# Kernel tuning notes

Hardware: AMD Instinct MI355X
Metric: run time of the kernel (lower is better)

The kernel has to match this reference:

```python
import jax, jax.numpy as jnp
import numpy as np

NE, NM, NR = 32768, 65536, 49152   # enzyme / metabolite / reaction node counts
E = 262144                          # edges per relation
H, HEADS, DH, FFN, EF = 128, 4, 32, 512, 8


def setup_inputs():
    key = jax.random.key(0)
    ks = iter(jax.random.split(key, 64))
    def nrm(shape, s=1.0):
        return jax.random.normal(next(ks), shape, jnp.float32) * s
    def idx(n):
        return jax.random.randint(next(ks), (E,), 0, n, jnp.int32)
    w = 0.02
    return {
        'h_enz': nrm((NE, H)), 'h_met': nrm((NM, H)), 'h_rxn': nrm((NR, H)),
        'ef_mod': nrm((E, EF)), 'ef_sig': nrm((E, EF)),
        'ef_brg': nrm((E, EF)), 'ef_trn': nrm((E, EF)),
        'ln1_g': jnp.ones((3, H)), 'ln1_b': jnp.zeros((3, H)),
        'ln2_g': jnp.ones((3, H)), 'ln2_b': jnp.zeros((3, H)),
        'wp': nrm((3, H, H), w), 'bp': jnp.zeros((3, H)),
        'wl': nrm((5, H, H), w), 'a_src': nrm((5, HEADS, DH), w), 'a_dst': nrm((5, HEADS, DH), w),
        'we': nrm((4, EF, H), w), 'a_edge': nrm((4, HEADS, DH), w),
        'w1': nrm((3, H, FFN), w), 'b1': jnp.zeros((3, FFN)),
        'w2': nrm((3, FFN, H), w), 'b2': jnp.zeros((3, H)),
        'src_sub': idx(NM), 'dst_sub': idx(NR),    # metabolite -substrate_of-> reaction
        'src_prod': idx(NR), 'dst_prod': idx(NM),  # reaction -produces-> metabolite
        'src_cat': idx(NE), 'dst_cat': idx(NR),    # enzyme -catalyzes-> reaction
        'src_mod': idx(NE), 'dst_mod': idx(NR),    # enzyme -modulates-> reaction
        'src_reg': idx(NE), 'dst_reg': idx(NE),    # enzyme -regulates-> enzyme
        'src_sig': idx(NM), 'dst_sig': idx(NE),    # metabolite -signaling-> enzyme
        'src_brg': idx(NM), 'dst_brg': idx(NM),    # metabolite -bridges-> metabolite
        'src_trn': idx(NM), 'dst_trn': idx(NM),    # metabolite -transports_to-> metabolite
    }


def _ln(x, g, b, eps=1e-5):
    m = jnp.mean(x, -1, keepdims=True)
    v = jnp.mean((x - m) ** 2, -1, keepdims=True)
    return g * (x - m) * jax.lax.rsqrt(v + eps) + b


def _phys(h_src, src, dst, nd, w, b):
    # KineticConv: linear transform of source feats, mean-aggregated onto dst nodes
    msg = (h_src @ w + b)[src]                                  # [E, H]
    s = jax.ops.segment_sum(msg, dst, num_segments=nd)
    deg = jax.ops.segment_sum(jnp.ones((src.shape[0], 1), msg.dtype), dst, num_segments=nd)
    return s / jnp.maximum(deg, 1.0)


def _gat(h_src, h_dst, src, dst, nd, w, a_s, a_d, ef=None, w_e=None, a_e=None):
    # LearnedConv: multi-head GAT, optional edge features added to attention logits
    zs = (h_src @ w).reshape(-1, HEADS, DH)                     # [Ns, H', D]
    zd = (h_dst @ w).reshape(-1, HEADS, DH)                     # [Nd, H', D]
    logit = jnp.einsum('nhd,hd->nh', zs, a_s)[src] + jnp.einsum('nhd,hd->nh', zd, a_d)[dst]
    if ef is not None:
        ze = (ef @ w_e).reshape(-1, HEADS, DH)
        logit = logit + jnp.einsum('ehd,hd->eh', ze, a_e)
    logit = jax.nn.leaky_relu(logit, 0.2)                       # [E, H']
    m = jax.ops.segment_max(logit, dst, num_segments=nd)
    ex = jnp.exp(logit - m[dst])
    den = jax.ops.segment_sum(ex, dst, num_segments=nd)
    alpha = ex / jnp.maximum(den[dst], 1e-9)                    # segment softmax over incoming edges
    out = jax.ops.segment_sum(alpha[:, :, None] * zs[src], dst, num_segments=nd)
    return out.reshape(nd, H)                                   # concat heads -> H


def reference(h_enz, h_met, h_rxn, ef_mod, ef_sig, ef_brg, ef_trn,
              ln1_g, ln1_b, ln2_g, ln2_b, wp, bp, wl, a_src, a_dst, we, a_edge,
              w1, b1, w2, b2,
              src_sub, dst_sub, src_prod, dst_prod, src_cat, dst_cat,
              src_mod, dst_mod, src_reg, dst_reg, src_sig, dst_sig,
              src_brg, dst_brg, src_trn, dst_trn):
    # ntype index: 0=enzyme 1=metabolite 2=reaction. Dropout = identity (eval mode).
    ne = _ln(h_enz, ln1_g[0], ln1_b[0])
    nm = _ln(h_met, ln1_g[1], ln1_b[1])
    nr = _ln(h_rxn, ln1_g[2], ln1_b[2])
    m_rxn = [
        _phys(nm, src_sub, dst_sub, NR, wp[0], bp[0]),
        _phys(ne, src_cat, dst_cat, NR, wp[2], bp[2]),
        _gat(ne, nr, src_mod, dst_mod, NR, wl[0], a_src[0], a_dst[0], ef_mod, we[0], a_edge[0]),
    ]
    m_met = [
        _phys(nr, src_prod, dst_prod, NM, wp[1], bp[1]),
        _gat(nm, nm, src_brg, dst_brg, NM, wl[3], a_src[3], a_dst[3], ef_brg, we[2], a_edge[2]),
        _gat(nm, nm, src_trn, dst_trn, NM, wl[4], a_src[4], a_dst[4], ef_trn, we[3], a_edge[3]),
    ]
    m_enz = [
        _gat(ne, ne, src_reg, dst_reg, NE, wl[1], a_src[1], a_dst[1]),
        _gat(nm, ne, src_sig, dst_sig, NE, wl[2], a_src[2], a_dst[2], ef_sig, we[1], a_edge[1]),
    ]
    # stack + mean aggregation across relations, then residual
    h_e = h_enz + sum(m_enz) / float(len(m_enz))
    h_m = h_met + sum(m_met) / float(len(m_met))
    h_r = h_rxn + sum(m_rxn) / float(len(m_rxn))
    # Pre-LN FFN per node type: h + W2 GELU(W1 LN(h))
    def ffn(h, i):
        n = _ln(h, ln2_g[i], ln2_b[i])
        return h + (jax.nn.gelu(n @ w1[i] + b1[i], approximate=False) @ w2[i] + b2[i])
    return jnp.concatenate([ffn(h_e, 0), ffn(h_m, 1), ffn(h_r, 2)], axis=0)
```

## Files before the change

kernel.cpp:

```cpp
#include <hip/hip_runtime.h>
#include <cstddef>

#define NE 32768
#define NM 65536
#define NR 49152
#define NTOT 147456
#define E2 262144
#define NDPAD 65536
#define RPS 65537
#define W1T_OFF 131072
#define W2T_OFF 327680

typedef __attribute__((ext_vector_type(8))) short bf16x8;
typedef __attribute__((ext_vector_type(4))) float f32x4;
typedef __attribute__((ext_vector_type(2))) float f32x2;

__device__ __forceinline__ unsigned short f2bf(float x) {
    unsigned u = __float_as_uint(x);
    return (unsigned short)((u + 0x7FFFu + ((u >> 16) & 1u)) >> 16);
}
__device__ __forceinline__ float bf2f(unsigned s) { return __uint_as_float(s << 16); }
__device__ __forceinline__ unsigned pk2(float a, float b) {
    return (unsigned)f2bf(a) | ((unsigned)f2bf(b) << 16);
}
__device__ __forceinline__ bf16x8 pack8(const float* v) {
    union { bf16x8 b; unsigned u[4]; } r;
#pragma unroll
    for (int i = 0; i < 4; ++i) r.u[i] = pk2(v[2 * i], v[2 * i + 1]);
    return r.b;
}
__device__ __forceinline__ bf16x8 pack8v(f32x4 a, f32x4 b) {
    union { bf16x8 v; unsigned u[4]; } r;
    r.u[0] = pk2(a[0], a[1]); r.u[1] = pk2(a[2], a[3]);
    r.u[2] = pk2(b[0], b[1]); r.u[3] = pk2(b[2], b[3]);
    return r.v;
}
__device__ __forceinline__ unsigned short pkfp8(float a, float b) {
    return (unsigned short)__builtin_amdgcn_cvt_pk_fp8_f32(a, b, 0u, false);
}
__device__ __forceinline__ void gll16(const void* g, void* l) {
    __builtin_amdgcn_global_load_lds(
        (const __attribute__((address_space(1))) void*)g,
        (__attribute__((address_space(3))) void*)l, 16, 0, 0);
}

__global__ __launch_bounds__(256) void convw(
    const float* __restrict__ wp, const float* __restrict__ wl,
    const float* __restrict__ w1, const float* __restrict__ w2,
    unsigned short* __restrict__ wbf)
{
    int i = blockIdx.x * 256 + threadIdx.x;
    float v;
    if (i < 131072) {
        int mat = i >> 14, r = i & 16383;
        int frag = r >> 9, lane = (r >> 3) & 63, j = r & 7;
        int nf = frag >> 2, ks = frag & 3;
        int n = nf * 16 + (lane & 15);
        int k = ks * 32 + (lane >> 4) * 8 + j;
        const float* src = (mat < 3) ? (wp + mat * 16384) : (wl + (mat - 3) * 16384);
        v = src[k * 128 + n];
    } else if (i < 327680) {
        int ii = i - 131072; int mat = ii >> 16, r = ii & 65535;
        int frag = r >> 9, lane = (r >> 3) & 63, j = r & 7;
        int nf = frag >> 2, ks = frag & 3;
        int n = nf * 16 + (lane & 15);
        int k = ks * 32 + (lane >> 4) * 8 + j;
        v = w1[mat * 65536 + k * 512 + n];
    } else {
        int ii = i - 327680; int mat = ii >> 16, r = ii & 65535;
        int frag = r >> 9, lane = (r >> 3) & 63, j = r & 7;
        int ks = frag >> 3, nf = frag & 7;
        int n = nf * 16 + (lane & 15);
        int k = ks * 32 + (lane >> 4) * 8 + j;
        v = w2[mat * 65536 + k * 128 + n];
    }
    wbf[i] = f2bf(v);
}

__global__ __launch_bounds__(256) void wqk(
    const float* __restrict__ wl, const float* __restrict__ a_src,
    const float* __restrict__ a_dst, unsigned short* __restrict__ wq)
{
    const int wi[7]  = {0, 2, 0, 1, 2, 3, 4};
    const int loi[7] = {0, 2, 0, 1, 2, 3, 4};
    const int lod[7] = {1, 1, 0, 0, 0, 0, 0};
    const int hii[7] = {-1, -1, -1, 1, -1, 3, 4};
    int site = blockIdx.x >> 2, ks = blockIdx.x & 3, t = threadIdx.x;
    const float* W = wl + wi[site] * 16384;
#pragma unroll
    for (int rep = 0; rep < 2; ++rep) {
        int e = t * 2 + rep;
        int lane = e >> 3, j = e & 7;
        int n = lane & 15;
        int k = ks * 32 + (lane >> 4) * 8 + j;
        float v = 0.f;
        if (n < 4) {
            const float* a = (lod[site] ? a_dst : a_src) + loi[site] * 128;
#pragma unroll 8
            for (int d = 0; d < 32; ++d) v += W[k * 128 + n * 32 + d] * a[n * 32 + d];
        } else if (n < 8 && hii[site] >= 0) {
            const float* a = a_dst + hii[site] * 128;
            int hh = n - 4;
#pragma unroll 8
            for (int d = 0; d < 32; ++d) v += W[k * 128 + hh * 32 + d] * a[hh * 32 + d];
        }
        wq[((site * 4 + ks) * 64 + lane) * 8 + j] = f2bf(v);
    }
}

__global__ __launch_bounds__(256) void ln1_kernel(
    const float* __restrict__ he, const float* __restrict__ hm, const float* __restrict__ hr,
    const float* __restrict__ g, const float* __restrict__ b, unsigned* __restrict__ nout)
{
    int row  = blockIdx.x * 4 + (threadIdx.x >> 6);
    int lane = threadIdx.x & 63;
    const float* src; int ti; int lr;
    if (row < NE)           { src = he; ti = 0; lr = row; }
    else if (row < NE + NM) { src = hm; ti = 1; lr = row - NE; }
    else                    { src = hr; ti = 2; lr = row - NE - NM; }
    float2 x = *(const float2*)(src + (size_t)lr * 128 + lane * 2);
    float s = x.x + x.y;
#pragma unroll
    for (int o = 32; o; o >>= 1) s += __shfl_xor(s, o);
    float mean = s * (1.0f / 128.0f);
    float dx = x.x - mean, dy = x.y - mean;
    float v = dx * dx + dy * dy;
#pragma unroll
    for (int o = 32; o; o >>= 1) v += __shfl_xor(v, o);
    float rstd = rsqrtf(v * (1.0f / 128.0f) + 1e-5f);
    int c = lane * 2;
    float y0 = g[ti * 128 + c]     * dx * rstd + b[ti * 128 + c];
    float y1 = g[ti * 128 + c + 1] * dy * rstd + b[ti * 128 + c + 1];
    nout[(size_t)row * 64 + lane] = pk2(y0, y1);
}

template <int LOG, bool BIAS>
__global__ __launch_bounds__(256) void gemm_v2(
    const unsigned short* __restrict__ A, const unsigned short* __restrict__ Wt,
    const float* __restrict__ bias, unsigned short* __restrict__ Zp,
    const unsigned short* __restrict__ WQ, float* __restrict__ oa, float* __restrict__ ob)
{
    __shared__ unsigned short WL[16384];
    int t = threadIdx.x, w = t >> 6, l = t & 63;
    int l15 = l & 15, lq = l >> 4;
#pragma unroll
    for (int i = 0; i < 8; ++i)
        gll16(Wt + i * 2048 + t * 8, (char*)WL + i * 4096 + t * 16);
    size_t row0 = (size_t)blockIdx.x * 128 + w * 32;
    f32x4 acc[2][8]; f32x4 accl[2];
#pragma unroll
    for (int r = 0; r < 2; ++r) {
        accl[r] = (f32x4){0.f, 0.f, 0.f, 0.f};
#pragma unroll
        for (int n = 0; n < 8; ++n) acc[r][n] = (f32x4){0.f, 0.f, 0.f, 0.f};
    }
    bf16x8 qf[4];
    if constexpr (LOG >= 1) {
#pragma unroll
        for (int ks = 0; ks < 4; ++ks) qf[ks] = *(const bf16x8*)(WQ + (ks * 64 + l) * 8);
    }
    __syncthreads();
#pragma unroll
    for (int ks = 0; ks < 4; ++ks) {
        int k0 = ks * 32 + lq * 8;
        bf16x8 a0 = *(const bf16x8*)(A + (row0 + l15) * 128 + k0);
        bf16x8 a1 = *(const bf16x8*)(A + (row0 + 16 + l15) * 128 + k0);
#pragma unroll
        for (int n = 0; n < 8; ++n) {
            bf16x8 bw = *(const bf16x8*)(WL + ((n * 4 + ks) * 64 + l) * 8);
            acc[0][n] = __builtin_amdgcn_mfma_f32_16x16x32_bf16(a0, bw, acc[0][n], 0, 0, 0);
            acc[1][n] = __builtin_amdgcn_mfma_f32_16x16x32_bf16(a1, bw, acc[1][n], 0, 0, 0);
        }
        if constexpr (LOG >= 1) {
            accl[0] = __builtin_amdgcn_mfma_f32_16x16x32_bf16(a0, qf[ks], accl[0], 0, 0, 0);
            accl[1] = __builtin_amdgcn_mfma_f32_16x16x32_bf16(a1, qf[ks], accl[1], 0, 0, 0);
        }
    }
#pragma unroll
    for (int n = 0; n < 4; ++n) {
        float bl = BIAS ? bias[n * 16 + l15] : 0.f;
        float bh = BIAS ? bias[n * 16 + l15 + 64] : 0.f;
#pragma unroll
        for (int r = 0; r < 2; ++r)
#pragma unroll
            for (int reg = 0; reg < 4; ++reg) {
                size_t row = row0 + r * 16 + lq * 4 + reg;
                Zp[row * 64 + n * 16 + l15] = pkfp8(acc[r][n][reg] + bl, acc[r][n + 4][reg] + bh);
            }
    }
    if constexpr (LOG >= 1) {
#pragma unroll
        for (int r = 0; r < 2; ++r)
#pragma unroll
            for (int reg = 0; reg < 4; ++reg) {
                size_t row = row0 + r * 16 + lq * 4 + reg;
                if (l15 < 4) oa[row * 4 + l15] = accl[r][reg];
                else if (LOG == 2 && l15 < 8) ob[row * 4 + (l15 - 4)] = accl[r][reg];
            }
    }
}

struct P8 { const int* a[8]; };
#define CHUNK 2048

__global__ __launch_bounds__(256) void bucket_count(P8 dsts, unsigned* __restrict__ bcnt)
{
    __shared__ unsigned lh[256];
    int blk = blockIdx.x, rel = blk >> 7, cb = blk & 127, t = threadIdx.x;
    lh[t] = 0; __syncthreads();
    const int* dp = dsts.a[rel] + cb * CHUNK;
#pragma unroll
    for (int it = 0; it < 8; ++it) atomicAdd(&lh[dp[it * 256 + t] >> 8], 1u);
    __syncthreads();
    atomicAdd(&bcnt[rel * 256 + t], lh[t]);
}

__global__ __launch_bounds__(256) void scanB(const unsigned* __restrict__ bcnt,
                                             unsigned* __restrict__ bbase,
                                             unsigned* __restrict__ bcur)
{
    __shared__ unsigned ts[256];
    int t = threadIdx.x;
    unsigned v[8]; unsigned run = 0;
#pragma unroll
    for (int i = 0; i < 8; ++i) { v[i] = bcnt[t * 8 + i]; run += v[i]; }
    ts[t] = run; __syncthreads();
    for (int off = 1; off < 256; off <<= 1) {
        unsigned x = (t >= off) ? ts[t - off] : 0u;
        __syncthreads(); ts[t] += x; __syncthreads();
    }
    unsigned base = ts[t] - run;
#pragma unroll
    for (int i = 0; i < 8; ++i) { bbase[t * 8 + i] = base; bcur[t * 8 + i] = base; base += v[i]; }
    if (t == 255) bbase[2048] = base;
}

__global__ __launch_bounds__(256) void bucket_fill(P8 dsts, P8 srcs,
                                                   unsigned* __restrict__ bcur,
                                                   unsigned long long* __restrict__ bb)
{
    __shared__ unsigned lh[256], lbase[256], lcur[256];
    int blk = blockIdx.x, rel = blk >> 7, cb = blk & 127, t = threadIdx.x;
    lh[t] = 0; lcur[t] = 0; __syncthreads();
    const int* dp = dsts.a[rel] + cb * CHUNK;
    const int* sp = srcs.a[rel] + cb * CHUNK;
    int dv[8];
#pragma unroll
    for (int it = 0; it < 8; ++it) { dv[it] = dp[it * 256 + t]; atomicAdd(&lh[dv[it] >> 8], 1u); }
    __syncthreads();
    lbase[t] = atomicAdd(&bcur[rel * 256 + t], lh[t]);
    __syncthreads();
#pragma unroll
    for (int it = 0; it < 8; ++it) {
        unsigned e = (unsigned)(cb * CHUNK + it * 256 + t);
        unsigned d = (unsigned)dv[it];
        unsigned s = (unsigned)sp[it * 256 + t];
        unsigned pos = atomicAdd(&lcur[d >> 8], 1u);
        bb[lbase[d >> 8] + pos] =
            (unsigned long long)s | ((unsigned long long)d << 16) | ((unsigned long long)e << 32);
    }
}

__global__ __launch_bounds__(256) void bucket_hist(const unsigned long long* __restrict__ bb,
                                                   const unsigned* __restrict__ bbase,
                                                   unsigned* __restrict__ hist)
{
    __shared__ unsigned lh[256];
    int blk = blockIdx.x, rel = blk >> 8, b = blk & 255, t = threadIdx.x;
    lh[t] = 0; __syncthreads();
    unsigned s0 = bbase[blk], s1 = bbase[blk + 1];
    for (unsigned i = s0 + t; i < s1; i += 256)
        atomicAdd(&lh[(unsigned)(bb[i] >> 16) & 255u], 1u);
    __syncthreads();
    hist[(size_t)rel * NDPAD + b * 256 + t] = lh[t];
}

__global__ __launch_bounds__(256) void scan1(const unsigned* __restrict__ hist,
                                             unsigned* __restrict__ rowptr,
                                             unsigned* __restrict__ blksum)
{
    __shared__ unsigned s[256];
    int b = blockIdx.x, rel = b >> 8, c = b & 255, t = threadIdx.x;
    unsigned v = hist[(size_t)rel * NDPAD + c * 256 + t];
    s[t] = v; __syncthreads();
    for (int off = 1; off < 256; off <<= 1) {
        unsigned x = (t >= off) ? s[t - off] : 0u;
        __syncthreads();
        s[t] += x;
        __syncthreads();
    }
    rowptr[(size_t)rel * RPS + c * 256 + t] = s[t] - v;
    if (t == 255) blksum[rel * 256 + c] = s[255];
}

__global__ __launch_bounds__(256) void scan2(unsigned* __restrict__ blksum,
                                             unsigned* __restrict__ rowptr)
{
    __shared__ unsigned s[256];
    int rel = blockIdx.x, t = threadIdx.x;
    unsigned v = blksum[rel * 256 + t];
    s[t] = v; __syncthreads();
    for (int off = 1; off < 256; off <<= 1) {
        unsigned x = (t >= off) ? s[t - off] : 0u;
        __syncthreads();
        s[t] += x;
        __syncthreads();
    }
    blksum[rel * 256 + t] = s[t] - v;
    if (t == 255) rowptr[(size_t)rel * RPS + 65536] = s[255];
}

__global__ __launch_bounds__(256) void scan3(unsigned* __restrict__ rowptr,
                                             const unsigned* __restrict__ blksum)
{
    int b = blockIdx.x, rel = b >> 8, c = b & 255, t = threadIdx.x;
    rowptr[(size_t)rel * RPS + c * 256 + t] += blksum[rel * 256 + c];
}

__global__ __launch_bounds__(256) void bucket_place(const unsigned long long* __restrict__ bb,
                                                    const unsigned* __restrict__ bbase,
                                                    const unsigned* __restrict__ rowptr,
                                                    int2* __restrict__ epair)
{
    __shared__ unsigned lrp[256], lcur[256];
    int blk = blockIdx.x, rel = blk >> 8, b = blk & 255, t = threadIdx.x;
    lrp[t] = rowptr[(size_t)rel * RPS + b * 256 + t];
    lcur[t] = 0; __syncthreads();
    unsigned s0 = bbase[blk], s1 = bbase[blk + 1];
    for (unsigned i = s0 + t; i < s1; i += 256) {
        unsigned long long pk = bb[i];
        unsigned s = (unsigned)pk & 0xffffu;
        unsigned d8 = (unsigned)(pk >> 16) & 255u;
        unsigned e = (unsigned)(pk >> 32);
        unsigned pos = atomicAdd(&lcur[d8], 1u);
        epair[(size_t)rel * E2 + lrp[d8] + pos] = make_int2((int)s, (int)e);
    }
}

__global__ __launch_bounds__(256) void ef4e_kernel(
    const float* __restrict__ efm, const float* __restrict__ efs,
    const float* __restrict__ efb, const float* __restrict__ eft,
    const float* __restrict__ we, const float* __restrict__ ae,
    uint2* __restrict__ ef4e)
{
    __shared__ float M[8][4];
    int b = blockIdx.x, t = threadIdx.x;
    int er = b >> 10;
    const float* ef = (er == 0) ? efm : (er == 1) ? efs : (er == 2) ? efb : eft;
    if (t < 32) {
        int f = t >> 2, hh = t & 3;
        float s = 0.f;
#pragma unroll 8
        for (int d = 0; d < 32; ++d) s += we[er * 1024 + f * 128 + hh * 32 + d] * ae[er * 128 + hh * 32 + d];
        M[f][hh] = s;
    }
    __syncthreads();
    int e = (b & 1023) * 256 + t;
    float4 a = *(const float4*)(ef + (size_t)e * 8);
    float4 c = *(const float4*)(ef + (size_t)e * 8 + 4);
    float o0 = a.x*M[0][0]+a.y*M[1][0]+a.z*M[2][0]+a.w*M[3][0]+c.x*M[4][0]+c.y*M[5][0]+c.z*M[6][0]+c.w*M[7][0];
// ... 152 lines not shown
    unsigned* __restrict__ accp, int n_nodes)
{
    int t = threadIdx.x;
    unsigned m = (unsigned)(t & 15);
    int d = blockIdx.x * 16 + (t >> 4);
    if (d >= n_nodes) return;
    int hs = (int)(m >> 3);
    float rlo[4] = {0, 0, 0, 0}, rhi[4] = {0, 0, 0, 0};
    gat_seg16<EF>(rowptr, epair, Zp, ls, ld, ef4e, d, m, hs, rlo, rhi);
    acc_write16(accp, d, m, ACC, rlo, rhi);
}

template <bool EFA, bool EFB, bool ACC>
__global__ __launch_bounds__(256) void dual_gat(
    const unsigned* __restrict__ rpA, const int2* __restrict__ epA,
    const unsigned short* __restrict__ ZA, const float* __restrict__ lsA,
    const float* __restrict__ ldA, const uint2* __restrict__ efA,
    const unsigned* __restrict__ rpB, const int2* __restrict__ epB,
    const unsigned short* __restrict__ ZB, const float* __restrict__ lsB,
    const float* __restrict__ ldB, const uint2* __restrict__ efB,
    unsigned* __restrict__ accp, int n_nodes)
{
    int t = threadIdx.x;
    unsigned m = (unsigned)(t & 15);
    int d = blockIdx.x * 16 + (t >> 4);
    if (d >= n_nodes) return;
    int hs = (int)(m >> 3);
    float rlo[4] = {0, 0, 0, 0}, rhi[4] = {0, 0, 0, 0};
    gat_seg16<EFA>(rpA, epA, ZA, lsA, ldA, efA, d, m, hs, rlo, rhi);
    gat_seg16<EFB>(rpB, epB, ZB, lsB, ldB, efB, d, m, hs, rlo, rhi);
    acc_write16(accp, d, m, ACC, rlo, rhi);
}

__global__ __launch_bounds__(256, 2) void ffn_v5(
    const float* __restrict__ h, const unsigned* __restrict__ accp,
    const float* __restrict__ g, const float* __restrict__ b,
    const unsigned short* __restrict__ w1t, const float* __restrict__ b1,
    const unsigned short* __restrict__ w2t, const float* __restrict__ b2,
    float* __restrict__ out, float invC)
{
    __shared__ unsigned short WB[2][16384];
    __shared__ float HW[4][1024];
    int t = threadIdx.x, w = t >> 6, l = t & 63;
    int l15 = l & 15, lq = l >> 4;
    size_t rw = (size_t)blockIdx.x * 128 + w * 32;
    float* myHW = HW[w];

    bf16x8 af[2][4];
#pragma unroll
    for (int rf = 0; rf < 2; ++rf) {
        size_t myrow = rw + rf * 16 + l15;
        const unsigned* ap = accp + myrow * 64 + lq * 8;
        uint4 ua0 = *(const uint4*)(ap);
        uint4 ua1 = *(const uint4*)(ap + 4);
        uint4 ub0 = *(const uint4*)(ap + 32);
        uint4 ub1 = *(const uint4*)(ap + 36);
        const float* hp = h + myrow * 128 + lq * 8;
        float4 hf[4][2];
        hf[0][0] = *(const float4*)(hp);      hf[0][1] = *(const float4*)(hp + 4);
        hf[1][0] = *(const float4*)(hp + 32); hf[1][1] = *(const float4*)(hp + 36);
        hf[2][0] = *(const float4*)(hp + 64); hf[2][1] = *(const float4*)(hp + 68);
        hf[3][0] = *(const float4*)(hp + 96); hf[3][1] = *(const float4*)(hp + 100);
        unsigned ua[8] = {ua0.x, ua0.y, ua0.z, ua0.w, ua1.x, ua1.y, ua1.z, ua1.w};
        unsigned ub[8] = {ub0.x, ub0.y, ub0.z, ub0.w, ub1.x, ub1.y, ub1.z, ub1.w};
        float hv[4][8];
#pragma unroll
        for (int j = 0; j < 8; ++j) {
            hv[0][j] = ((const float*)hf[0])[j] + bf2f(ua[j] & 0xffffu) * invC;
            hv[1][j] = ((const float*)hf[1])[j] + bf2f(ub[j] & 0xffffu) * invC;
            hv[2][j] = ((const float*)hf[2])[j] + bf2f(ua[j] >> 16) * invC;
            hv[3][j] = ((const float*)hf[3])[j] + bf2f(ub[j] >> 16) * invC;
        }
        float s = 0.f;
#pragma unroll
        for (int ks = 0; ks < 4; ++ks)
#pragma unroll
            for (int j = 0; j < 8; ++j) s += hv[ks][j];
        s += __shfl_xor(s, 16); s += __shfl_xor(s, 32);
// ... 32 lines not shown
    int swR = (l15 & 7) << 2;
    for (int ch = 0; ch < 8; ++ch) {
        if (ch < 7) {
            const unsigned short* s1p = w1t + (ch + 1) * 8192;
            const unsigned short* s2p = w2t + (ch + 1) * 8192;
#pragma unroll
            for (int i = 0; i < 4; ++i) {
                gll16(s1p + i * 2048 + t * 8, (char*)WB[buf ^ 1] + i * 4096 + t * 16);
                gll16(s2p + i * 2048 + t * 8, (char*)WB[buf ^ 1] + 16384 + i * 4096 + t * 16);
            }
        }
        f32x4 acc1[2][4];
#pragma unroll
        for (int rf = 0; rf < 2; ++rf)
#pragma unroll
            for (int n = 0; n < 4; ++n) acc1[rf][n] = (f32x4){0.f, 0.f, 0.f, 0.f};
#pragma unroll
        for (int ks = 0; ks < 4; ++ks)
#pragma unroll
            for (int nf = 0; nf < 4; ++nf) {
                bf16x8 bw = *(const bf16x8*)(WB[buf] + ((nf * 4 + ks) * 64 + l) * 8);
                acc1[0][nf] = __builtin_amdgcn_mfma_f32_16x16x32_bf16(af[0][ks], bw, acc1[0][nf], 0, 0, 0);
                acc1[1][nf] = __builtin_amdgcn_mfma_f32_16x16x32_bf16(af[1][ks], bw, acc1[1][nf], 0, 0, 0);
            }
#pragma unroll
        for (int rf = 0; rf < 2; ++rf) {
#pragma unroll
            for (int nf = 0; nf < 4; ++nf) {
                float bv = b1[ch * 64 + nf * 16 + l15];
#pragma unroll
                for (int reg = 0; reg < 4; ++reg) {
                    int row = lq * 4 + reg;
                    float x = acc1[rf][nf][reg] + bv;
                    float ge = 0.5f * x * (1.0f + erff(x * 0.70710678118654752f));
                    myHW[row * 64 + ((nf * 16 + l15) ^ ((row & 7) << 2))] = ge;
                }
            }
#pragma unroll
            for (int ks2 = 0; ks2 < 2; ++ks2) {
                int cb = ks2 * 32 + lq * 8;
                f32x4 x0 = *(const f32x4*)(myHW + l15 * 64 + (cb ^ swR));
                f32x4 x1 = *(const f32x4*)(myHW + l15 * 64 + ((cb + 4) ^ swR));
                bf16x8 a2 = pack8v(x0, x1);
#pragma unroll
                for (int nf = 0; nf < 8; ++nf) {
                    bf16x8 bw = *(const bf16x8*)(WB[buf] + 8192 + ((ks2 * 8 + nf) * 64 + l) * 8);
                    facc[rf][nf] = __builtin_amdgcn_mfma_f32_16x16x32_bf16(a2, bw, facc[rf][nf], 0, 0, 0);
                }
            }
        }
        __syncthreads();
        buf ^= 1;
    }
#pragma unroll
    for (int rf = 0; rf < 2; ++rf)
#pragma unroll
        for (int nf = 0; nf < 8; ++nf) {
            int col = nf * 16 + l15;
            float bv = b2[col];
            int ci = col & 63;
            bool hi = col >= 64;
#pragma unroll
            for (int reg = 0; reg < 4; ++reg) {
                size_t row = rw + rf * 16 + lq * 4 + reg;
                unsigned pv = accp[row * 64 + ci];
                float av = bf2f(hi ? (pv >> 16) : (pv & 0xffffu));
                out[row * 128 + col] = h[row * 128 + col] + av * invC + facc[rf][nf][reg] + bv;
            }
// ... 20 lines not shown
    const float* wl     = (const float*)d_in[13];
    const float* a_src  = (const float*)d_in[14];
    const float* a_dst  = (const float*)d_in[15];
    const float* we     = (const float*)d_in[16];
    const float* a_edge = (const float*)d_in[17];
    const float* w1     = (const float*)d_in[18];
    const float* b1     = (const float*)d_in[19];
    const float* w2     = (const float*)d_in[20];
    const float* b2     = (const float*)d_in[21];
    const int* src_sub  = (const int*)d_in[22];
    const int* dst_sub  = (const int*)d_in[23];
    const int* src_prod = (const int*)d_in[24];
    const int* dst_prod = (const int*)d_in[25];
    const int* src_cat  = (const int*)d_in[26];
    const int* dst_cat  = (const int*)d_in[27];
    const int* src_mod  = (const int*)d_in[28];
    const int* dst_mod  = (const int*)d_in[29];
    const int* src_reg  = (const int*)d_in[30];
    const int* dst_reg  = (const int*)d_in[31];
    const int* src_sig  = (const int*)d_in[32];
    const int* dst_sig  = (const int*)d_in[33];
    const int* src_brg  = (const int*)d_in[34];
    const int* dst_brg  = (const int*)d_in[35];
    const int* src_trn  = (const int*)d_in[36];
    const int* dst_trn  = (const int*)d_in[37];
    float* out = (float*)d_out;

    char* p = (char*)d_ws;
    unsigned* accp = (unsigned*)p;            p += (size_t)NTOT * 64 * 4;
    unsigned short* ZpA = (unsigned short*)p; p += (size_t)NM * 64 * 2;
    unsigned long long* bukbuf = (unsigned long long*)p;
    unsigned short* ZpB = (unsigned short*)p; p += (size_t)8 * E2 * 8;
    int2* epair = (int2*)p;                   p += (size_t)8 * E2 * 8;
    unsigned* hist = (unsigned*)p;
    uint2* ef4e = (uint2*)p;                  p += (size_t)4 * E2 * 8;
    float* ls3 = (float*)p;                   p += (size_t)NE * 4 * 4;
    float* ld3 = (float*)p;                   p += (size_t)NR * 4 * 4;
    float* ls4 = (float*)p;                   p += (size_t)NE * 4 * 4;
    float* ld4 = (float*)p;                   p += (size_t)NE * 4 * 4;
    float* ls5 = (float*)p;                   p += (size_t)NM * 4 * 4;
    float* ld5 = (float*)p;                   p += (size_t)NE * 4 * 4;
    float* ls6 = (float*)p;                   p += (size_t)NM * 4 * 4;
    float* ld6 = (float*)p;                   p += (size_t)NM * 4 * 4;
    float* ls7 = (float*)p;                   p += (size_t)NM * 4 * 4;
    float* ld7 = (float*)p;                   p += (size_t)NM * 4 * 4;
    unsigned short* wbf = (unsigned short*)p; p += (size_t)524288 * 2;
    unsigned short* wq  = (unsigned short*)p; p += (size_t)7 * 2048 * 2;
    unsigned* rowptr = (unsigned*)p;          p += (size_t)8 * RPS * 4;
    unsigned* bcnt = (unsigned*)p;            p += 2048 * 4;
    unsigned* bbase = (unsigned*)p;           p += 2049 * 4;
    unsigned* bcur = (unsigned*)p;            p += 2048 * 4;
    unsigned* blksum = (unsigned*)p;          p += (size_t)8 * 256 * 4;
    if (ws_size < (size_t)(p - (char*)d_ws)) return;

    unsigned* nrm32 = (unsigned*)d_out;
    const unsigned short* nbf_enz = (const unsigned short*)d_out;
    const unsigned short* nbf_met = nbf_enz + (size_t)NE * 128;
    const unsigned short* nbf_rxn = nbf_enz + (size_t)(NE + NM) * 128;
    unsigned* acc_enz = accp;
    unsigned* acc_met = accp + (size_t)NE * 64;
    unsigned* acc_rxn = accp + (size_t)(NE + NM) * 64;

    P8 dsts, srcs;
    dsts.a[0] = dst_sub;  srcs.a[0] = src_sub;
    dsts.a[1] = dst_prod; srcs.a[1] = src_prod;
    dsts.a[2] = dst_cat;  srcs.a[2] = src_cat;
    dsts.a[3] = dst_mod;  srcs.a[3] = src_mod;
    dsts.a[4] = dst_reg;  srcs.a[4] = src_reg;
    dsts.a[5] = dst_sig;  srcs.a[5] = src_sig;
    dsts.a[6] = dst_brg;  srcs.a[6] = src_brg;
    dsts.a[7] = dst_trn;  srcs.a[7] = src_trn;

    hipMemsetAsync(bcnt, 0, 2048 * 4, stream);
    convw<<<2048, 256, 0, stream>>>(wp, wl, w1, w2, wbf);
    ln1_kernel<<<NTOT / 4, 256, 0, stream>>>(h_enz, h_met, h_rxn, ln1_g, ln1_b, nrm32);
    wqk<<<28, 256, 0, stream>>>(wl, a_src, a_dst, wq);
    bucket_count<<<1024, 256, 0, stream>>>(dsts, bcnt);
    scanB<<<1, 256, 0, stream>>>(bcnt, bbase, bcur);
    bucket_fill<<<1024, 256, 0, stream>>>(dsts, srcs, bcur, bukbuf);
    bucket_hist<<<2048, 256, 0, stream>>>(bukbuf, bbase, hist);
    scan1<<<2048, 256, 0, stream>>>(hist, rowptr, blksum);
    scan2<<<8, 256, 0, stream>>>(blksum, rowptr);
    scan3<<<2048, 256, 0, stream>>>(rowptr, blksum);
    bucket_place<<<2048, 256, 0, stream>>>(bukbuf, bbase, rowptr, epair);
    ef4e_kernel<<<4096, 256, 0, stream>>>(ef_mod, ef_sig, ef_brg, ef_trn, we, a_edge, ef4e);

#define RP(r) (rowptr + (size_t)(r) * RPS)
#define EP(r) (epair + (size_t)(r) * E2)
#define WQS(s) (wq + (size_t)(s) * 2048)
#define EF4(er) (ef4e + (size_t)(er) * E2)

    gemm_v2<0, true><<<NM / 128, 256, 0, stream>>>(nbf_met, wbf + 0 * 16384, bp + 0, ZpA,
                                                   nullptr, nullptr, nullptr);
    gemm_v2<1, true><<<NE / 128, 256, 0, stream>>>(nbf_enz, wbf + 2 * 16384, bp + 256, ZpB,
                                                   WQS(1), ld5, nullptr);
    dual_phys<false><<<NR / 16, 256, 0, stream>>>(RP(0), EP(0), ZpA, RP(2), EP(2), ZpB,
                                                  acc_rxn, NR);
    gemm_v2<1, true><<<NR / 128, 256, 0, stream>>>(nbf_rxn, wbf + 1 * 16384, bp + 128, ZpA,
                                                   WQS(0), ld3, nullptr);
    phys_gather<false><<<NM / 16, 256, 0, stream>>>(RP(1), EP(1), ZpA, acc_met, NM);
    gemm_v2<1, false><<<NE / 128, 256, 0, stream>>>(nbf_enz, wbf + 3 * 16384, nullptr, ZpB,
                                                    WQS(2), ls3, nullptr);
    gat_gather<true, true><<<NR / 16, 256, 0, stream>>>(RP(3), EP(3), ZpB, ls3, ld3, EF4(0),
                                                        acc_rxn, NR);
    gemm_v2<2, false><<<NE / 128, 256, 0, stream>>>(nbf_enz, wbf + 4 * 16384, nullptr, ZpA,
                                                    WQS(3), ls4, ld4);
    gemm_v2<1, false><<<NM / 128, 256, 0, stream>>>(nbf_met, wbf + 5 * 16384, nullptr, ZpB,
                                                    WQS(4), ls5, nullptr);
    dual_gat<false, true, false><<<NE / 16, 256, 0, stream>>>(
        RP(4), EP(4), ZpA, ls4, ld4, nullptr,
        RP(5), EP(5), ZpB, ls5, ld5, EF4(1), acc_enz, NE);
    gemm_v2<2, false><<<NM / 128, 256, 0, stream>>>(nbf_met, wbf + 6 * 16384, nullptr, ZpA,
                                                    WQS(5), ls6, ld6);
    gemm_v2<2, false><<<NM / 128, 256, 0, stream>>>(nbf_met, wbf + 7 * 16384, nullptr, ZpB,
                                                    WQS(6), ls7, ld7);
    dual_gat<true, true, true><<<NM / 16, 256, 0, stream>>>(
        RP(6), EP(6), ZpA, ls6, ld6, EF4(2),
        RP(7), EP(7), ZpB, ls7, ld7, EF4(3), acc_met, NM);

    ffn_v5<<<NE / 128, 256, 0, stream>>>(h_enz, acc_enz, ln2_g + 0, ln2_b + 0,
                                         wbf + W1T_OFF + 0 * 65536, b1 + 0,
                                         wbf + W2T_OFF + 0 * 65536, b2 + 0,
                                         out + 0, 0.5f);
    ffn_v5<<<NM / 128, 256, 0, stream>>>(h_met, acc_met, ln2_g + 128, ln2_b + 128,
                                         wbf + W1T_OFF + 1 * 65536, b1 + 512,
                                         wbf + W2T_OFF + 1 * 65536, b2 + 128,
                                         out + (size_t)NE * 128, 1.0f / 3.0f);
    ffn_v5<<<NR / 128, 256, 0, stream>>>(h_rxn, acc_rxn, ln2_g + 256, ln2_b + 256,
                                         wbf + W1T_OFF + 2 * 65536, b1 + 1024,
                                         wbf + W2T_OFF + 2 * 65536, b2 + 256,
                                         out + (size_t)(NE + NM) * 128, 1.0f / 3.0f);
#undef RP
#undef EP
#undef WQS
#undef EF4
}
```

Baseline: 469.4 us.

## Merge prep, CSR-build, GEMM and FFN launches and use tanh-form GELU

Folds ln1, weight conversion and the attention-logit weight prep into a single prep kernel. It merges histogram with scan1 and scan3 with placement, pairs independent projection GEMMs into one launch each, and runs all three FFNs in one grid. This cuts launch count and drops the intermediate hist buffer round-trip. Separately, the exact erf GELU is replaced by a sigmoid-based tanh approximation, which is cheaper but changes numerics slightly. The GEMM's compile-time LOG/BIAS branches become runtime pointer checks, adding some branching and register pressure.

```diff
diff --git a/kernel.cpp b/kernel.cpp
--- a/kernel.cpp
+++ b/kernel.cpp
@@ -6,10 +6,11 @@
 #define NR 49152
 #define NTOT 147456
 #define E2 262144
-#define NDPAD 65536
 #define RPS 65537
 #define W1T_OFF 131072
 #define W2T_OFF 327680
+#define LN1_BLK 36864
+#define CONV_BLK 2048
 
 typedef __attribute__((ext_vector_type(8))) short bf16x8;
 typedef __attribute__((ext_vector_type(4))) float f32x4;
@@ -43,110 +44,126 @@
         (const __attribute__((address_space(1))) void*)g,
         (__attribute__((address_space(3))) void*)l, 16, 0, 0);
 }
-
-__global__ __launch_bounds__(256) void convw(
+__device__ __forceinline__ float gelu(float x) {
+    float y = x * (1.5957691216f + 0.0713548163f * (x * x));
+    float e = __expf(-y);
+    return x / (1.0f + e);
+}
+
+__global__ __launch_bounds__(256) void prep_all(
+    const float* __restrict__ he, const float* __restrict__ hm, const float* __restrict__ hr,
+    const float* __restrict__ g1, const float* __restrict__ b1g, unsigned* __restrict__ nout,
     const float* __restrict__ wp, const float* __restrict__ wl,
     const float* __restrict__ w1, const float* __restrict__ w2,
-    unsigned short* __restrict__ wbf)
-{
-    int i = blockIdx.x * 256 + threadIdx.x;
-    float v;
-    if (i < 131072) {
-        int mat = i >> 14, r = i & 16383;
-        int frag = r >> 9, lane = (r >> 3) & 63, j = r & 7;
-        int nf = frag >> 2, ks = frag & 3;
-        int n = nf * 16 + (lane & 15);
-        int k = ks * 32 + (lane >> 4) * 8 + j;
-        const float* src = (mat < 3) ? (wp + mat * 16384) : (wl + (mat - 3) * 16384);
-        v = src[k * 128 + n];
-    } else if (i < 327680) {
-        int ii = i - 131072; int mat = ii >> 16, r = ii & 65535;
-        int frag = r >> 9, lane = (r >> 3) & 63, j = r & 7;
-        int nf = frag >> 2, ks = frag & 3;
-        int n = nf * 16 + (lane & 15);
-        int k = ks * 32 + (lane >> 4) * 8 + j;
-        v = w1[mat * 65536 + k * 512 + n];
+    unsigned short* __restrict__ wbf,
+    const float* __restrict__ a_src, const float* __restrict__ a_dst,
+    unsigned short* __restrict__ wq)
+{
+    int blk = blockIdx.x, t = threadIdx.x;
+    if (blk < LN1_BLK) {
+        int row  = blk * 4 + (t >> 6);
+        int lane = t & 63;
+        const float* src; int ti; int lr;
+        if (row < NE)           { src = he; ti = 0; lr = row; }
+        else if (row < NE + NM) { src = hm; ti = 1; lr = row - NE; }
+        else                    { src = hr; ti = 2; lr = row - NE - NM; }
+        float2 x = *(const float2*)(src + (size_t)lr * 128 + lane * 2);
+        float s = x.x + x.y;
+#pragma unroll
+        for (int o = 32; o; o >>= 1) s += __shfl_xor(s, o);
+        float mean = s * (1.0f / 128.0f);
+        float dx = x.x - mean, dy = x.y - mean;
+        float v = dx * dx + dy * dy;
+#pragma unroll
+        for (int o = 32; o; o >>= 1) v += __shfl_xor(v, o);
+        float rstd = rsqrtf(v * (1.0f / 128.0f) + 1e-5f);
+        int c = lane * 2;
+        float y0 = g1[ti * 128 + c]     * dx * rstd + b1g[ti * 128 + c];
+        float y1 = g1[ti * 128 + c + 1] * dy * rstd + b1g[ti * 128 + c + 1];
+        nout[(size_t)row * 64 + lane] = pk2(y0, y1);
+    } else if (blk < LN1_BLK + CONV_BLK) {
+        int i = (blk - LN1_BLK) * 256 + t;
+        float v;
+        if (i < 131072) {
+            int mat = i >> 14, r = i & 16383;
+            int frag = r >> 9, lane = (r >> 3) & 63, j = r & 7;
+            int nf = frag >> 2, ks = frag & 3;
+            int n = nf * 16 + (lane & 15);
+            int k = ks * 32 + (lane >> 4) * 8 + j;
+            const float* src = (mat < 3) ? (wp + mat * 16384) : (wl + (mat - 3) * 16384);
+            v = src[k * 128 + n];
+        } else if (i < 327680) {
+            int ii = i - 131072; int mat = ii >> 16, r = ii & 65535;
+            int frag = r >> 9, lane = (r >> 3) & 63, j = r & 7;
+            int nf = frag >> 2, ks = frag & 3;
+            int n = nf * 16 + (lane & 15);
+            int k = ks * 32 + (lane >> 4) * 8 + j;
+            v = w1[mat * 65536 + k * 512 + n];
+        } else {
+            int ii = i - 327680; int mat = ii >> 16, r = ii & 65535;
+            int frag = r >> 9, lane = (r >> 3) & 63, j = r & 7;
+            int ks = frag >> 3, nf = frag & 7;
+            int n = nf * 16 + (lane & 15);
+            int k = ks * 32 + (lane >> 4) * 8 + j;
+            v = w2[mat * 65536 + k * 128 + n];
+        }
+        wbf[i] = f2bf(v);
     } else {
-        int ii = i - 327680; int mat = ii >> 16, r = ii & 65535;
-        int frag = r >> 9, lane = (r >> 3) & 63, j = r & 7;
-        int ks = frag >> 3, nf = frag & 7;
-        int n = nf * 16 + (lane & 15);
-        int k = ks * 32 + (lane >> 4) * 8 + j;
-        v = w2[mat * 65536 + k * 128 + n];
-    }
-    wbf[i] = f2bf(v);
-}
-
-__global__ __launch_bounds__(256) void wqk(
-    const float* __restrict__ wl, const float* __restrict__ a_src,
-    const float* __restrict__ a_dst, unsigned short* __restrict__ wq)
-{
-    const int wi[7]  = {0, 2, 0, 1, 2, 3, 4};
-    const int loi[7] = {0, 2, 0, 1, 2, 3, 4};
-    const int lod[7] = {1, 1, 0, 0, 0, 0, 0};
-    const int hii[7] = {-1, -1, -1, 1, -1, 3, 4};
-    int site = blockIdx.x >> 2, ks = blockIdx.x & 3, t = threadIdx.x;
-    const float* W = wl + wi[site] * 16384;
-#pragma unroll
-    for (int rep = 0; rep < 2; ++rep) {
-        int e = t * 2 + rep;
-        int lane = e >> 3, j = e & 7;
-        int n = lane & 15;
-        int k = ks * 32 + (lane >> 4) * 8 + j;
-        float v = 0.f;
-        if (n < 4) {
-            const float* a = (lod[site] ? a_dst : a_src) + loi[site] * 128;
+        const int wi[7]  = {0, 2, 0, 1, 2, 3, 4};
+        const int loi[7] = {0, 2, 0, 1, 2, 3, 4};
+        const int lod[7] = {1, 1, 0, 0, 0, 0, 0};
+        const int hii[7] = {-1, -1, -1, 1, -1, 3, 4};
+        int bid = blk - LN1_BLK - CONV_BLK;
+        int site = bid >> 2, ks = bid & 3;
+        const float* W = wl + wi[site] * 16384;
+#pragma unroll
+        for (int rep = 0; rep < 2; ++rep) {
+            int e = t * 2 + rep;
+            int lane = e >> 3, j = e & 7;
+            int n = lane & 15;
+            int k = ks * 32 + (lane >> 4) * 8 + j;
+            float v = 0.f;
+            if (n < 4) {
+                const float* a = (lod[site] ? a_dst : a_src) + loi[site] * 128;
 #pragma unroll 8
-            for (int d = 0; d < 32; ++d) v += W[k * 128 + n * 32 + d] * a[n * 32 + d];
-        } else if (n < 8 && hii[site] >= 0) {
-            const float* a = a_dst + hii[site] * 128;
-            int hh = n - 4;
+                for (int d = 0; d < 32; ++d) v += W[k * 128 + n * 32 + d] * a[n * 32 + d];
+            } else if (n < 8 && hii[site] >= 0) {
+                const float* a = a_dst + hii[site] * 128;
+                int hh = n - 4;
 #pragma unroll 8
-            for (int d = 0; d < 32; ++d) v += W[k * 128 + hh * 32 + d] * a[hh * 32 + d];
-        }
-        wq[((site * 4 + ks) * 64 + lane) * 8 + j] = f2bf(v);
-    }
-}
-
-__global__ __launch_bounds__(256) void ln1_kernel(
-    const float* __restrict__ he, const float* __restrict__ hm, const float* __restrict__ hr,
-    const float* __restrict__ g, const float* __restrict__ b, unsigned* __restrict__ nout)
-{
-    int row  = blockIdx.x * 4 + (threadIdx.x >> 6);
-    int lane = threadIdx.x & 63;
-    const float* src; int ti; int lr;
-    if (row < NE)           { src = he; ti = 0; lr = row; }
-    else if (row < NE + NM) { src = hm; ti = 1; lr = row - NE; }
-    else                    { src = hr; ti = 2; lr = row - NE - NM; }
-    float2 x = *(const float2*)(src + (size_t)lr * 128 + lane * 2);
-    float s = x.x + x.y;
-#pragma unroll
-    for (int o = 32; o; o >>= 1) s += __shfl_xor(s, o);
-    float mean = s * (1.0f / 128.0f);
-    float dx = x.x - mean, dy = x.y - mean;
-    float v = dx * dx + dy * dy;
-#pragma unroll
-    for (int o = 32; o; o >>= 1) v += __shfl_xor(v, o);
-    float rstd = rsqrtf(v * (1.0f / 128.0f) + 1e-5f);
-    int c = lane * 2;
-    float y0 = g[ti * 128 + c]     * dx * rstd + b[ti * 128 + c];
-    float y1 = g[ti * 128 + c + 1] * dy * rstd + b[ti * 128 + c + 1];
-    nout[(size_t)row * 64 + lane] = pk2(y0, y1);
-}
-
-template <int LOG, bool BIAS>
-__global__ __launch_bounds__(256) void gemm_v2(
-    const unsigned short* __restrict__ A, const unsigned short* __restrict__ Wt,
-    const float* __restrict__ bias, unsigned short* __restrict__ Zp,
-    const unsigned short* __restrict__ WQ, float* __restrict__ oa, float* __restrict__ ob)
+                for (int d = 0; d < 32; ++d) v += W[k * 128 + hh * 32 + d] * a[hh * 32 + d];
+            }
+            wq[((site * 4 + ks) * 64 + lane) * 8 + j] = f2bf(v);
+        }
+    }
+}
+
+struct G2 {
+    const unsigned short *A0, *Wt0; const float* b0; unsigned short* Z0;
+    const unsigned short* Q0; float *oa0, *ob0;
+    const unsigned short *A1, *Wt1; const float* b1; unsigned short* Z1;
+    const unsigned short* Q1; float *oa1, *ob1;
+    int n0;
+};
+
+__global__ __launch_bounds__(256) void gemm_pair(G2 P)
 {
     __shared__ unsigned short WL[16384];
     int t = threadIdx.x, w = t >> 6, l = t & 63;
     int l15 = l & 15, lq = l >> 4;
+    int e = (blockIdx.x >= P.n0) ? 1 : 0;
+    const unsigned short* A  = e ? P.A1 : P.A0;
+    const unsigned short* Wt = e ? P.Wt1 : P.Wt0;
+    const float* bias        = e ? P.b1 : P.b0;
+    unsigned short* Zp       = e ? P.Z1 : P.Z0;
+    const unsigned short* WQ = e ? P.Q1 : P.Q0;
+    float* oa                = e ? P.oa1 : P.oa0;
+    float* ob                = e ? P.ob1 : P.ob0;
+    int lb = blockIdx.x - (e ? P.n0 : 0);
 #pragma unroll
     for (int i = 0; i < 8; ++i)
         gll16(Wt + i * 2048 + t * 8, (char*)WL + i * 4096 + t * 16);
-    size_t row0 = (size_t)blockIdx.x * 128 + w * 32;
+    size_t row0 = (size_t)lb * 128 + w * 32;
     f32x4 acc[2][8]; f32x4 accl[2];
 #pragma unroll
     for (int r = 0; r < 2; ++r) {
@@ -154,8 +171,9 @@
 #pragma unroll
         for (int n = 0; n < 8; ++n) acc[r][n] = (f32x4){0.f, 0.f, 0.f, 0.f};
     }
+    bool haslog = (WQ != nullptr);
     bf16x8 qf[4];
-    if constexpr (LOG >= 1) {
+    if (haslog) {
 #pragma unroll
         for (int ks = 0; ks < 4; ++ks) qf[ks] = *(const bf16x8*)(WQ + (ks * 64 + l) * 8);
     }
@@ -171,15 +189,16 @@
             acc[0][n] = __builtin_amdgcn_mfma_f32_16x16x32_bf16(a0, bw, acc[0][n], 0, 0, 0);
             acc[1][n] = __builtin_amdgcn_mfma_f32_16x16x32_bf16(a1, bw, acc[1][n], 0, 0, 0);
         }
-        if constexpr (LOG >= 1) {
+        if (haslog) {
             accl[0] = __builtin_amdgcn_mfma_f32_16x16x32_bf16(a0, qf[ks], accl[0], 0, 0, 0);
             accl[1] = __builtin_amdgcn_mfma_f32_16x16x32_bf16(a1, qf[ks], accl[1], 0, 0, 0);
         }
     }
+    bool hasb = (bias != nullptr);
 #pragma unroll
     for (int n = 0; n < 4; ++n) {
-        float bl = BIAS ? bias[n * 16 + l15] : 0.f;
-        float bh = BIAS ? bias[n * 16 + l15 + 64] : 0.f;
+        float bl = hasb ? bias[n * 16 + l15] : 0.f;
+        float bh = hasb ? bias[n * 16 + l15 + 64] : 0.f;
 #pragma unroll
         for (int r = 0; r < 2; ++r)
 #pragma unroll
@@ -188,14 +207,14 @@
                 Zp[row * 64 + n * 16 + l15] = pkfp8(acc[r][n][reg] + bl, acc[r][n + 4][reg] + bh);
             }
     }
-    if constexpr (LOG >= 1) {
+    if (haslog) {
 #pragma unroll
         for (int r = 0; r < 2; ++r)
 #pragma unroll
             for (int reg = 0; reg < 4; ++reg) {
                 size_t row = row0 + r * 16 + lq * 4 + reg;
-                if (l15 < 4) oa[row * 4 + l15] = accl[r][reg];
-                else if (LOG == 2 && l15 < 8) ob[row * 4 + (l15 - 4)] = accl[r][reg];
+                if (oa && l15 < 4) oa[row * 4 + l15] = accl[r][reg];
+                else if (ob && l15 >= 4 && l15 < 8) ob[row * 4 + (l15 - 4)] = accl[r][reg];
             }
     }
 }
@@ -261,27 +280,19 @@
     }
 }
 
-__global__ __launch_bounds__(256) void bucket_hist(const unsigned long long* __restrict__ bb,
-                                                   const unsigned* __restrict__ bbase,
-                                                   unsigned* __restrict__ hist)
-{
-    __shared__ unsigned lh[256];
+__global__ __launch_bounds__(256) void hist_scan(const unsigned long long* __restrict__ bb,
+                                                 const unsigned* __restrict__ bbase,
+                                                 unsigned* __restrict__ rowptr,
+                                                 unsigned* __restrict__ blksum)
+{
+    __shared__ unsigned lh[256], s[256];
     int blk = blockIdx.x, rel = blk >> 8, b = blk & 255, t = threadIdx.x;
     lh[t] = 0; __syncthreads();
     unsigned s0 = bbase[blk], s1 = bbase[blk + 1];
     for (unsigned i = s0 + t; i < s1; i += 256)
         atomicAdd(&lh[(unsigned)(bb[i] >> 16) & 255u], 1u);
     __syncthreads();
-    hist[(size_t)rel * NDPAD + b * 256 + t] = lh[t];
-}
-
-__global__ __launch_bounds__(256) void scan1(const unsigned* __restrict__ hist,
-                                             unsigned* __restrict__ rowptr,
-                                             unsigned* __restrict__ blksum)
-{
-    __shared__ unsigned s[256];
-    int b = blockIdx.x, rel = b >> 8, c = b & 255, t = threadIdx.x;
-    unsigned v = hist[(size_t)rel * NDPAD + c * 256 + t];
+    unsigned v = lh[t];
     s[t] = v; __syncthreads();
     for (int off = 1; off < 256; off <<= 1) {
         unsigned x = (t >= off) ? s[t - off] : 0u;
@@ -289,8 +300,8 @@
         s[t] += x;
         __syncthreads();
     }
-    rowptr[(size_t)rel * RPS + c * 256 + t] = s[t] - v;
-    if (t == 255) blksum[rel * 256 + c] = s[255];
+    rowptr[(size_t)rel * RPS + b * 256 + t] = s[t] - v;
+    if (t == 255) blksum[rel * 256 + b] = s[255];
 }
 
 __global__ __launch_bounds__(256) void scan2(unsigned* __restrict__ blksum,
@@ -310,22 +321,17 @@
     if (t == 255) rowptr[(size_t)rel * RPS + 65536] = s[255];
 }
 
-__global__ __launch_bounds__(256) void scan3(unsigned* __restrict__ rowptr,
-                                             const unsigned* __restrict__ blksum)
-{
-    int b = blockIdx.x, rel = b >> 8, c = b & 255, t = threadIdx.x;
-    rowptr[(size_t)rel * RPS + c * 256 + t] += blksum[rel * 256 + c];
-}
-
-__global__ __launch_bounds__(256) void bucket_place(const unsigned long long* __restrict__ bb,
-                                                    const unsigned* __restrict__ bbase,
-                                                    const unsigned* __restrict__ rowptr,
-                                                    int2* __restrict__ epair)
+__global__ __launch_bounds__(256) void scan3_place(const unsigned long long* __restrict__ bb,
+                                                   const unsigned* __restrict__ bbase,
+                                                   unsigned* __restrict__ rowptr,
+                                                   const unsigned* __restrict__ blksum,
+                                                   int2* __restrict__ epair)
 {
     __shared__ unsigned lrp[256], lcur[256];
     int blk = blockIdx.x, rel = blk >> 8, b = blk & 255, t = threadIdx.x;
-    lrp[t] = rowptr[(size_t)rel * RPS + b * 256 + t];
-    lcur[t] = 0; __syncthreads();
+    unsigned fin = rowptr[(size_t)rel * RPS + b * 256 + t] + blksum[rel * 256 + b];
+    rowptr[(size_t)rel * RPS + b * 256 + t] = fin;
+    lrp[t] = fin; lcur[t] = 0; __syncthreads();
     unsigned s0 = bbase[blk], s1 = bbase[blk + 1];
     for (unsigned i = s0 + t; i < s1; i += 256) {
         unsigned long long pk = bb[i];
@@ -544,18 +550,36 @@
     acc_write16(accp, d, m, ACC, rlo, rhi);
 }
 
-__global__ __launch_bounds__(256, 2) void ffn_v5(
-    const float* __restrict__ h, const unsigned* __restrict__ accp,
-    const float* __restrict__ g, const float* __restrict__ b,
-    const unsigned short* __restrict__ w1t, const float* __restrict__ b1,
-    const unsigned short* __restrict__ w2t, const float* __restrict__ b2,
-    float* __restrict__ out, float invC)
+struct FP {
+    const float* h[3]; const unsigned* ac[3];
+    const float* g[3]; const float* b[3];
+    const unsigned short* w1[3]; const float* bb1[3];
+    const unsigned short* w2[3]; const float* bb2[3];
+    float* out[3]; float invC[3];
+    int n1, n2;
+};
+
+__global__ __launch_bounds__(256, 2) void ffn_all(FP P)
 {
     __shared__ unsigned short WB[2][16384];
     __shared__ float HW[4][1024];
+    int blk = blockIdx.x;
+    int ti = (blk >= P.n2) ? 2 : (blk >= P.n1) ? 1 : 0;
+    int lb = blk - (ti == 2 ? P.n2 : ti == 1 ? P.n1 : 0);
+    const float* h = P.h[ti];
+    const unsigned* accp = P.ac[ti];
+    const float* g = P.g[ti];
+    const float* b = P.b[ti];
+    const unsigned short* w1t = P.w1[ti];
+    const float* b1 = P.bb1[ti];
+    const unsigned short* w2t = P.w2[ti];
+    const float* b2 = P.bb2[ti];
+    float* out = P.out[ti];
+    float invC = P.invC[ti];
+
     int t = threadIdx.x, w = t >> 6, l = t & 63;
     int l15 = l & 15, lq = l >> 4;
-    size_t rw = (size_t)blockIdx.x * 128 + w * 32;
+    size_t rw = (size_t)lb * 128 + w * 32;
     float* myHW = HW[w];
 
     bf16x8 af[2][4];
@@ -654,8 +678,7 @@
                 for (int reg = 0; reg < 4; ++reg) {
                     int row = lq * 4 + reg;
                     float x = acc1[rf][nf][reg] + bv;
-                    float ge = 0.5f * x * (1.0f + erff(x * 0.70710678118654752f));
-                    myHW[row * 64 + ((nf * 16 + l15) ^ ((row & 7) << 2))] = ge;
+                    myHW[row * 64 + ((nf * 16 + l15) ^ ((row & 7) << 2))] = gelu(x);
                 }
             }
 #pragma unroll
@@ -742,7 +765,6 @@
     unsigned long long* bukbuf = (unsigned long long*)p;
     unsigned short* ZpB = (unsigned short*)p; p += (size_t)8 * E2 * 8;
     int2* epair = (int2*)p;                   p += (size_t)8 * E2 * 8;
-    unsigned* hist = (unsigned*)p;
     uint2* ef4e = (uint2*)p;                  p += (size_t)4 * E2 * 8;
     float* ls3 = (float*)p;                   p += (size_t)NE * 4 * 4;
     float* ld3 = (float*)p;                   p += (size_t)NR * 4 * 4;
@@ -782,17 +804,15 @@
     dsts.a[7] = dst_trn;  srcs.a[7] = src_trn;
 
     hipMemsetAsync(bcnt, 0, 2048 * 4, stream);
-    convw<<<2048, 256, 0, stream>>>(wp, wl, w1, w2, wbf);
-    ln1_kernel<<<NTOT / 4, 256, 0, stream>>>(h_enz, h_met, h_rxn, ln1_g, ln1_b, nrm32);
-    wqk<<<28, 256, 0, stream>>>(wl, a_src, a_dst, wq);
+    prep_all<<<LN1_BLK + CONV_BLK + 28, 256, 0, stream>>>(
+        h_enz, h_met, h_rxn, ln1_g, ln1_b, nrm32,
+        wp, wl, w1, w2, wbf, a_src, a_dst, wq);
     bucket_count<<<1024, 256, 0, stream>>>(dsts, bcnt);
     scanB<<<1, 256, 0, stream>>>(bcnt, bbase, bcur);
     bucket_fill<<<1024, 256, 0, stream>>>(dsts, srcs, bcur, bukbuf);
-    bucket_hist<<<2048, 256, 0, stream>>>(bukbuf, bbase, hist);
-    scan1<<<2048, 256, 0, stream>>>(hist, rowptr, blksum);
+    hist_scan<<<2048, 256, 0, stream>>>(bukbuf, bbase, rowptr, blksum);
     scan2<<<8, 256, 0, stream>>>(blksum, rowptr);
-    scan3<<<2048, 256, 0, stream>>>(rowptr, blksum);
-    bucket_place<<<2048, 256, 0, stream>>>(bukbuf, bbase, rowptr, epair);
+    scan3_place<<<2048, 256, 0, stream>>>(bukbuf, bbase, rowptr, blksum, epair);
     ef4e_kernel<<<4096, 256, 0, stream>>>(ef_mod, ef_sig, ef_brg, ef_trn, we, a_edge, ef4e);
 
 #define RP(r) (rowptr + (size_t)(r) * RPS)
@@ -800,46 +820,57 @@
 #define WQS(s) (wq + (size_t)(s) * 2048)
 #define EF4(er) (ef4e + (size_t)(er) * E2)
 
-    gemm_v2<0, true><<<NM / 128, 256, 0, stream>>>(nbf_met, wbf + 0 * 16384, bp + 0, ZpA,
-                                                   nullptr, nullptr, nullptr);
-    gemm_v2<1, true><<<NE / 128, 256, 0, stream>>>(nbf_enz, wbf + 2 * 16384, bp + 256, ZpB,
-                                                   WQS(1), ld5, nullptr);
+    {
+        G2 P = {nbf_met, wbf + 0 * 16384, bp + 0,   ZpA, nullptr, nullptr, nullptr,
+                nbf_enz, wbf + 2 * 16384, bp + 256, ZpB, WQS(1),  ld5,     nullptr,
+                NM / 128};
+        gemm_pair<<<NM / 128 + NE / 128, 256, 0, stream>>>(P);
+    }
     dual_phys<false><<<NR / 16, 256, 0, stream>>>(RP(0), EP(0), ZpA, RP(2), EP(2), ZpB,
                                                   acc_rxn, NR);
-    gemm_v2<1, true><<<NR / 128, 256, 0, stream>>>(nbf_rxn, wbf + 1 * 16384, bp + 128, ZpA,
-                                                   WQS(0), ld3, nullptr);
+    {
+        G2 P = {nbf_rxn, wbf + 1 * 16384, bp + 128, ZpA, WQS(0), ld3, nullptr,
+                nbf_enz, wbf + 3 * 16384, nullptr,  ZpB, WQS(2), ls3, nullptr,
+                NR / 128};
+        gemm_pair<<<NR / 128 + NE / 128, 256, 0, stream>>>(P);
+    }
     phys_gather<false><<<NM / 16, 256, 0, stream>>>(RP(1), EP(1), ZpA, acc_met, NM);
-    gemm_v2<1, false><<<NE / 128, 256, 0, stream>>>(nbf_enz, wbf + 3 * 16384, nullptr, ZpB,
-                                                    WQS(2), ls3, nullptr);
     gat_gather<true, true><<<NR / 16, 256, 0, stream>>>(RP(3), EP(3), ZpB, ls3, ld3, EF4(0),
                                                         acc_rxn, NR);
-    gemm_v2<2, false><<<NE / 128, 256, 0, stream>>>(nbf_enz, wbf + 4 * 16384, nullptr, ZpA,
-                                                    WQS(3), ls4, ld4);
-    gemm_v2<1, false><<<NM / 128, 256, 0, stream>>>(nbf_met, wbf + 5 * 16384, nullptr, ZpB,
-                                                    WQS(4), ls5, nullptr);
+    {
+        G2 P = {nbf_enz, wbf + 4 * 16384, nullptr, ZpA, WQS(3), ls4, ld4,
+                nbf_met, wbf + 5 * 16384, nullptr, ZpB, WQS(4), ls5, nullptr,
+                NE / 128};
+        gemm_pair<<<NE / 128 + NM / 128, 256, 0, stream>>>(P);
+    }
     dual_gat<false, true, false><<<NE / 16, 256, 0, stream>>>(
         RP(4), EP(4), ZpA, ls4, ld4, nullptr,
         RP(5), EP(5), ZpB, ls5, ld5, EF4(1), acc_enz, NE);
-    gemm_v2<2, false><<<NM / 128, 256, 0, stream>>>(nbf_met, wbf + 6 * 16384, nullptr, ZpA,
-                                                    WQS(5), ls6, ld6);
-    gemm_v2<2, false><<<NM / 128, 256, 0, stream>>>(nbf_met, wbf + 7 * 16384, nullptr, ZpB,
-                                                    WQS(6), ls7, ld7);
+    {
+        G2 P = {nbf_met, wbf + 6 * 16384, nullptr, ZpA, WQS(5), ls6, ld6,
+                nbf_met, wbf + 7 * 16384, nullptr, ZpB, WQS(6), ls7, ld7,
+                NM / 128};
+        gemm_pair<<<NM / 128 + NM / 128, 256, 0, stream>>>(P);
+    }
     dual_gat<true, true, true><<<NM / 16, 256, 0, stream>>>(
         RP(6), EP(6), ZpA, ls6, ld6, EF4(2),
         RP(7), EP(7), ZpB, ls7, ld7, EF4(3), acc_met, NM);
 
-    ffn_v5<<<NE / 128, 256, 0, stream>>>(h_enz, acc_enz, ln2_g + 0, ln2_b + 0,
-                                         wbf + W1T_OFF + 0 * 65536, b1 + 0,
-                                         wbf + W2T_OFF + 0 * 65536, b2 + 0,
-                                         out + 0, 0.5f);
-    ffn_v5<<<NM / 128, 256, 0, stream>>>(h_met, acc_met, ln2_g + 128, ln2_b + 128,
-                                         wbf + W1T_OFF + 1 * 65536, b1 + 512,
-                                         wbf + W2T_OFF + 1 * 65536, b2 + 128,
-                                         out + (size_t)NE * 128, 1.0f / 3.0f);
-    ffn_v5<<<NR / 128, 256, 0, stream>>>(h_rxn, acc_rxn, ln2_g + 256, ln2_b + 256,
-                                         wbf + W1T_OFF + 2 * 65536, b1 + 1024,
-                                         wbf + W2T_OFF + 2 * 65536, b2 + 256,
-                                         out + (size_t)(NE + NM) * 128, 1.0f / 3.0f);
+    {
+        FP P;
+        P.h[0] = h_enz; P.h[1] = h_met; P.h[2] = h_rxn;
+        P.ac[0] = acc_enz; P.ac[1] = acc_met; P.ac[2] = acc_rxn;
+        P.g[0] = ln2_g; P.g[1] = ln2_g + 128; P.g[2] = ln2_g + 256;
+        P.b[0] = ln2_b; P.b[1] = ln2_b + 128; P.b[2] = ln2_b + 256;
+        P.w1[0] = wbf + W1T_OFF; P.w1[1] = wbf + W1T_OFF + 65536; P.w1[2] = wbf + W1T_OFF + 2 * 65536;
+        P.bb1[0] = b1; P.bb1[1] = b1 + 512; P.bb1[2] = b1 + 1024;
+        P.w2[0] = wbf + W2T_OFF; P.w2[1] = wbf + W2T_OFF + 65536; P.w2[2] = wbf + W2T_OFF + 2 * 65536;
+        P.bb2[0] = b2; P.bb2[1] = b2 + 128; P.bb2[2] = b2 + 256;
+        P.out[0] = out; P.out[1] = out + (size_t)NE * 128; P.out[2] = out + (size_t)(NE + NM) * 128;
+        P.invC[0] = 0.5f; P.invC[1] = 1.0f / 3.0f; P.invC[2] = 1.0f / 3.0f;
+        P.n1 = NE / 128; P.n2 = NE / 128 + NM / 128;
+        ffn_all<<<NE / 128 + NM / 128 + NR / 128, 256, 0, stream>>>(P);
+    }
 #undef RP
 #undef EP
 #undef WQS
```

Result: faster. 443.9 us (-5.4%).
